# Kernel optimization log

Hardware: AMD Instinct MI355X
Metric: run time of the kernel (lower is better)

The kernel has to match this reference:

```python
import jax, jax.numpy as jnp
import numpy as np
import math

DIM = 4096
N_HEADS = 32
HEAD_DIM = DIM // N_HEADS
BSZ = 2
SEQLEN = 2048
MAX_SEQ = 2048


def _make_freqs_cis(seqlen, head_dim, theta=10000.0):
    # (seqlen, head_dim//2, 2) packed as (cos, sin) pairs, like complex rotary freqs
    inv = 1.0 / (theta ** (np.arange(0, head_dim, 2).astype(np.float32) / head_dim))
    t = np.arange(seqlen, dtype=np.float32)
    ang = np.outer(t, inv)  # (seqlen, head_dim//2)
    return jnp.asarray(np.stack([np.cos(ang), np.sin(ang)], axis=-1))


def setup_inputs() -> dict:
    key = jax.random.key(0)
    ks = jax.random.split(key, 6)
    scale = 1.0 / math.sqrt(DIM)
    x = jax.random.normal(ks[0], (BSZ, SEQLEN, DIM), dtype=jnp.float32)
    wq = jax.random.normal(ks[1], (DIM, DIM), dtype=jnp.float32) * scale
    wk = jax.random.normal(ks[2], (DIM, DIM), dtype=jnp.float32) * scale
    wv = jax.random.normal(ks[3], (DIM, DIM), dtype=jnp.float32) * scale
    wo = jax.random.normal(ks[4], (DIM, DIM), dtype=jnp.float32) * scale
    freqs_cis = _make_freqs_cis(SEQLEN, HEAD_DIM)
    # causal mask (1,1,S,S): 0 on/below diagonal, large negative above
    mask = jnp.triu(jnp.full((SEQLEN, SEQLEN), -1e9, dtype=jnp.float32), k=1)[None, None]
    hidden_state = jnp.zeros((2, BSZ, MAX_SEQ, N_HEADS, HEAD_DIM), dtype=jnp.float32)
    return {"x": x, "freqs_cis": freqs_cis, "mask": mask, "hidden_state": hidden_state,
            "wq": wq, "wk": wk, "wv": wv, "wo": wo, "start_pos": 0}


def _apply_rotary(x, freqs_cis):
    # x: (b, s, h, d); freqs_cis: (s, d//2, 2) as (cos, sin)
    b, s, h, d = x.shape
    xr = x.astype(jnp.float32).reshape(b, s, h, d // 2, 2)
    fc = freqs_cis.reshape(1, s, 1, d // 2, 2)
    real = xr[..., 0] * fc[..., 0] - xr[..., 1] * fc[..., 1]
    imag = xr[..., 0] * fc[..., 1] + xr[..., 1] * fc[..., 0]
    return jnp.stack([real, imag], axis=-1).reshape(b, s, h, d).astype(x.dtype)


def reference(x, freqs_cis, mask, hidden_state, wq, wk, wv, wo, start_pos):
    bsz, seqlen, dim = x.shape
    h, hd = N_HEADS, HEAD_DIM
    xq = (x @ wq.T).reshape(bsz, seqlen, h, hd)
    xk = (x @ wk.T).reshape(bsz, seqlen, h, hd)
    xv = (x @ wv.T).reshape(bsz, seqlen, h, hd)
    xq = _apply_rotary(xq, freqs_cis)
    xk = _apply_rotary(xk, freqs_cis)
    # KV-cache write at static start_pos
    new_k = hidden_state[0].at[:bsz, start_pos:start_pos + seqlen].set(xk)
    new_v = hidden_state[1].at[:bsz, start_pos:start_pos + seqlen].set(xv)
    new_hidden = jnp.stack([new_k, new_v], axis=0)
    keys = new_k[:bsz, :start_pos + seqlen]      # (b, kv, h, hd)
    values = new_v[:bsz, :start_pos + seqlen]
    # attention
    scores = jnp.einsum('bqhd,bkhd->bhqk', xq, keys) / math.sqrt(hd)
    scores = scores + mask
    probs = jax.nn.softmax(scores.astype(jnp.float32), axis=-1).astype(xq.dtype)
    out = jnp.einsum('bhqk,bkhd->bqhd', probs, values).reshape(bsz, seqlen, h * hd)
    return out @ wo.T, new_hidden
```

## Files before the change

kernel.cpp:

```cpp
#include <hip/hip_runtime.h>
#include <hip/hip_bf16.h>

#define DIM   4096
#define SEQ   2048
#define NH    32
#define HD    128
#define BSZ   2
#define SEG   16777216

typedef unsigned short u16;
typedef unsigned int   u32;
typedef __attribute__((ext_vector_type(8))) short bf16x8;
typedef __attribute__((ext_vector_type(4))) float f32x4;
typedef __attribute__((ext_vector_type(4))) u16   u16x4;

__device__ __forceinline__ float b2f(u16 u) {
    union { u32 i; float f; } c; c.i = ((u32)u) << 16; return c.f;
}
__device__ __forceinline__ u16 f2b(float f) {
    u32 x = __float_as_uint(f);
    return (u16)((x + 0x7FFFu + ((x >> 16) & 1u)) >> 16);
}
__device__ __forceinline__ void gload_lds16(const void* g, void* l) {
    __builtin_amdgcn_global_load_lds(
        (__attribute__((address_space(1))) void*)(unsigned long)(g),
        (__attribute__((address_space(3))) void*)(l), 16, 0, 0);
}

__global__ __launch_bounds__(256) void cast5(const float* __restrict__ x,
                                             const float* __restrict__ wq,
                                             const float* __restrict__ wk,
                                             const float* __restrict__ wv,
                                             const float* __restrict__ wo,
                                             u16* __restrict__ dst) {
    int i = blockIdx.x * 1024 + threadIdx.x * 4;
    int seg = i >> 24;
    int off = i & (SEG - 1);
    const float* s = x;
    if (seg == 1) s = wq; else if (seg == 2) s = wk;
    else if (seg == 3) s = wv; else if (seg == 4) s = wo;
    float4 v = *(const float4*)(s + off);
    u16x4 o; o.x = f2b(v.x); o.y = f2b(v.y); o.z = f2b(v.z); o.w = f2b(v.w);
    *(u16x4*)(dst + i) = o;
}

template<int OUT_BF16>
__global__ __launch_bounds__(256) void gemm_bt(const u16* __restrict__ A,
                                               const u16* __restrict__ Bbase,
                                               void* __restrict__ Cv) {
    __shared__ __align__(16) u16 smem[8192];
    const int tid = threadIdx.x;
    const int lane = tid & 63, w = tid >> 6;
    const int quad = lane >> 4, m16 = lane & 15;
    const int m0 = blockIdx.y * 128, n0 = blockIdx.x * 128;
    const int wm = (w & 1) * 64, wn = (w >> 1) * 64;
    const u16* B = Bbase + (size_t)blockIdx.z * SEG;

    f32x4 acc[4][4];
    for (int a = 0; a < 4; ++a) for (int b = 0; b < 4; ++b) acc[a][b] = 0.f;

    const int gbase = w * 256 + lane;

    for (int k0 = 0; k0 < DIM; k0 += 32) {
        __syncthreads();
        for (int j = 0; j < 4; ++j) {
            int g = gbase + j * 64;
            int row = (g >> 2) & 127;
            int ch = (g & 3) ^ ((row >> 1) & 3);
            const u16* src = (g < 512 ? A + (m0 + row) * DIM : B + (n0 + row) * DIM)
                             + k0 + ch * 8;
            gload_lds16(src, (char*)smem + w * 4096 + j * 1024);
        }
        __syncthreads();

        bf16x8 af[4], bfr[4];
        for (int mt = 0; mt < 4; ++mt) {
            int row = wm + mt * 16 + m16;
            int ch = quad ^ ((row >> 1) & 3);
            af[mt] = *(const bf16x8*)(smem + row * 32 + ch * 8);
        }
        for (int nt = 0; nt < 4; ++nt) {
            int row = wn + nt * 16 + m16;
            int ch = quad ^ ((row >> 1) & 3);
            bfr[nt] = *(const bf16x8*)(smem + 4096 + row * 32 + ch * 8);
        }
        for (int mt = 0; mt < 4; ++mt)
            for (int nt = 0; nt < 4; ++nt)
                acc[mt][nt] = __builtin_amdgcn_mfma_f32_16x16x32_bf16(
                    af[mt], bfr[nt], acc[mt][nt], 0, 0, 0);
    }

    for (int mt = 0; mt < 4; ++mt) for (int nt = 0; nt < 4; ++nt) {
        int row = m0 + wm + mt * 16 + quad * 4;
        int col = n0 + wn + nt * 16 + m16;
        if (OUT_BF16) {
            u16* C = (u16*)Cv + (size_t)blockIdx.z * SEG;
            for (int r = 0; r < 4; ++r) C[(row + r) * DIM + col] = f2b(acc[mt][nt][r]);
        } else {
            float* C = (float*)Cv + (size_t)blockIdx.z * SEG;
            for (int r = 0; r < 4; ++r) C[(row + r) * DIM + col] = acc[mt][nt][r];
        }
    }
}

__global__ __launch_bounds__(256) void rope(const u16* __restrict__ XQ,
                                            const u16* __restrict__ XK,
                                            const float* __restrict__ FC,
                                            u16* __restrict__ Qo,
                                            u16* __restrict__ Ko,
                                            float* __restrict__ KH) {
    int tid = blockIdx.x * 256 + threadIdx.x;
    int i = tid & 63;
    int s = (tid >> 11) & 2047;
    float2 cs = *(const float2*)(FC + (s * 64 + i) * 2);
    u32 q = ((const u32*)XQ)[tid];
    u32 k = ((const u32*)XK)[tid];
    float q0 = b2f((u16)(q & 0xffff)), q1 = b2f((u16)(q >> 16));
    float k0 = b2f((u16)(k & 0xffff)), k1 = b2f((u16)(k >> 16));
    float qr = q0 * cs.x - q1 * cs.y, qi = q0 * cs.y + q1 * cs.x;
    float kr = k0 * cs.x - k1 * cs.y, ki = k0 * cs.y + k1 * cs.x;
    ((u32*)Qo)[tid] = (u32)f2b(qr) | ((u32)f2b(qi) << 16);
    ((u32*)Ko)[tid] = (u32)f2b(kr) | ((u32)f2b(ki) << 16);
    *(float2*)(KH + (size_t)tid * 2) = make_float2(kr, ki);
}

__global__ __launch_bounds__(256) void vprep(const u16* __restrict__ XV,
                                             float* __restrict__ VH,
                                             u16* __restrict__ VT) {
    __shared__ u16 tile[64][65];
    int bs = blockIdx.x;
    int bd = blockIdx.y;
    int bh = blockIdx.z;
    int b = bh >> 5, h = bh & 31;
    int t = threadIdx.x;
    int c = t & 63, r4 = t >> 6;
    for (int i = 0; i < 16; ++i) {
        int sr = i * 4 + r4;
        int gi = ((b * SEQ + bs * 64 + sr) * NH + h) * HD + bd * 64 + c;
        u16 v = XV[gi];
        VH[gi] = b2f(v);
        tile[sr][c] = v;
    }
    __syncthreads();
    for (int i = 0; i < 16; ++i) {
        int dr = i * 4 + r4;
        VT[(bh * HD + bd * 64 + dr) * SEQ + bs * 64 + c] = tile[c][dr];
    }
}

__global__ __launch_bounds__(256, 2) void flash(const u16* __restrict__ Q,
                                                const u16* __restrict__ K,
                                                const u16* __restrict__ Vt,
                                                u16* __restrict__ O) {
    __shared__ __align__(16) u16 k_lds[64 * 128];
    __shared__ __align__(16) u16 v_lds[128 * 64];
    __shared__ __align__(16) u16 p_lds[4][32 * 68];

    const int tid = threadIdx.x, lane = tid & 63, w = tid >> 6;
    const int quad = lane >> 4, m16 = lane & 15;
    const int bh = blockIdx.x;
    const int b = bh >> 5, h = bh & 31;
    const int qt = (gridDim.y - 1) - blockIdx.y;
    const int q0 = qt * 128;
    const int wrow = q0 + w * 32;

    const int gk = w * 256 + lane;
    bf16x8 qa[2][4];
#pragma unroll
    for (int mt = 0; mt < 2; ++mt) {
        const u16* qp = Q + ((size_t)(b * SEQ + wrow + mt * 16 + m16) * NH + h) * HD;
#pragma unroll
        for (int ks = 0; ks < 4; ++ks) qa[mt][ks] = *(const bf16x8*)(qp + ks * 32 + quad * 8);
    }

    float mi[2][4], li[2][4];
    f32x4 o[2][8];
#pragma unroll
    for (int mt = 0; mt < 2; ++mt)
#pragma unroll
        for (int r = 0; r < 4; ++r) { mi[mt][r] = -1e30f; li[mt][r] = 0.f; }
#pragma unroll
    for (int mt = 0; mt < 2; ++mt)
#pragma unroll
        for (int n = 0; n < 8; ++n) o[mt][n] = 0.f;

    const float scale = 0.08838834764831845f;
    const int nkt = 2 * qt + 2;

    const u16* Kbase = K + ((size_t)(b * SEQ) * NH + h) * HD;
    const u16* Vbase = Vt + (size_t)(bh * HD) * SEQ;

    for (int kt = 0; kt < nkt; ++kt) {
        const int k0 = kt * 64;
        __syncthreads();
#pragma unroll
        for (int j = 0; j < 4; ++j) {
            int g = gk + j * 64;
            int r = g >> 4, p = g & 15, c = p ^ (r & 15);
            gload_lds16(Kbase + (size_t)(k0 + r) * DIM + c * 8,
                        (char*)k_lds + w * 4096 + j * 1024);
        }
#pragma unroll
        for (int j = 0; j < 4; ++j) {
            int g = gk + j * 64;
            int r = g >> 3, p = g & 7, c = p ^ (r & 7);
            gload_lds16(Vbase + (size_t)r * SEQ + k0 + c * 8,
                        (char*)v_lds + w * 4096 + j * 1024);
        }
        __syncthreads();

        if (k0 > wrow + 31) continue;

        f32x4 s[2][4];
#pragma unroll
        for (int mt = 0; mt < 2; ++mt)
#pragma unroll
            for (int nt = 0; nt < 4; ++nt) s[mt][nt] = 0.f;
#pragma unroll
        for (int ks = 0; ks < 4; ++ks)
#pragma unroll
            for (int nt = 0; nt < 4; ++nt) {
                int rk = nt * 16 + m16;
                int p = (ks * 4 + quad) ^ m16;
                bf16x8 kb = *(const bf16x8*)(k_lds + rk * 128 + p * 8);
#pragma unroll
                for (int mt = 0; mt < 2; ++mt)
                    s[mt][nt] = __builtin_amdgcn_mfma_f32_16x16x32_bf16(
                        qa[mt][ks], kb, s[mt][nt], 0, 0, 0);
            }

#pragma unroll
        for (int mt = 0; mt < 2; ++mt) {
            float sv[4][4];
            const bool need_mask = (k0 + 63) > (wrow + mt * 16);
#pragma unroll
            for (int nt = 0; nt < 4; ++nt)
#pragma unroll
                for (int r = 0; r < 4; ++r) {
                    float v = s[mt][nt][r] * scale;
                    if (need_mask) {
                        int col = k0 + nt * 16 + m16;
                        int rq = wrow + mt * 16 + quad * 4 + r;
                        if (col > rq) v = -1e30f;
                    }
                    sv[nt][r] = v;
                }
#pragma unroll
            for (int r = 0; r < 4; ++r) {
                float mx = fmaxf(fmaxf(sv[0][r], sv[1][r]), fmaxf(sv[2][r], sv[3][r]));
#pragma unroll
                for (int off = 8; off >= 1; off >>= 1) mx = fmaxf(mx, __shfl_xor(mx, off));
                float mnew = fmaxf(mi[mt][r], mx);
                float alpha = __expf(mi[mt][r] - mnew);
                float sum = 0.f;
#pragma unroll
                for (int nt = 0; nt < 4; ++nt) {
                    float pv = __expf(sv[nt][r] - mnew);
                    sum += pv;
                    p_lds[w][(mt * 16 + quad * 4 + r) * 68 + nt * 16 + m16] = f2b(pv);
                }
#pragma unroll
                for (int off = 8; off >= 1; off >>= 1) sum += __shfl_xor(sum, off);
                li[mt][r] = li[mt][r] * alpha + sum;
                mi[mt][r] = mnew;
#pragma unroll
                for (int n8 = 0; n8 < 8; ++n8) o[mt][n8][r] *= alpha;
            }
        }

        asm volatile("s_waitcnt lgkmcnt(0)" ::: "memory");

#pragma unroll
        for (int ks2 = 0; ks2 < 2; ++ks2) {
            bf16x8 pa[2];
#pragma unroll
            for (int mt = 0; mt < 2; ++mt)
                pa[mt] = *(const bf16x8*)(&p_lds[w][0] + (mt * 16 + m16) * 68 + ks2 * 32 + quad * 8);
#pragma unroll
            for (int n8 = 0; n8 < 8; ++n8) {
                int rv = n8 * 16 + m16;
                int p = (ks2 * 4 + quad) ^ (m16 & 7);
                bf16x8 vb = *(const bf16x8*)(v_lds + rv * 64 + p * 8);
#pragma unroll
                for (int mt = 0; mt < 2; ++mt)
                    o[mt][n8] = __builtin_amdgcn_mfma_f32_16x16x32_bf16(
                        pa[mt], vb, o[mt][n8], 0, 0, 0);
            }
        }
    }

#pragma unroll
    for (int mt = 0; mt < 2; ++mt) {
        float inv[4];
#pragma unroll
        for (int r = 0; r < 4; ++r) inv[r] = 1.0f / li[mt][r];
#pragma unroll
        for (int n8 = 0; n8 < 8; ++n8)
#pragma unroll
            for (int r = 0; r < 4; ++r) {
                int rq = wrow + mt * 16 + quad * 4 + r;
                O[((size_t)(b * SEQ + rq) * NH + h) * HD + n8 * 16 + m16] =
                    f2b(o[mt][n8][r] * inv[r]);
            }
    }
}

extern "C" void kernel_launch(void* const* d_in, const int* in_sizes, int n_in,
                              void* d_out, int out_size, void* d_ws, size_t ws_size,
                              hipStream_t stream) {
    const float* x  = (const float*)d_in[0];
    const float* fc = (const float*)d_in[1];
    const float* wq = (const float*)d_in[4];
    const float* wk = (const float*)d_in[5];
    const float* wv = (const float*)d_in[6];
    const float* wo = (const float*)d_in[7];

    float* out = (float*)d_out;
    float* kh  = out + 16777216;
    float* vh  = out + 33554432;

    u16* ws = (u16*)d_ws;
    u16* xb  = ws + 0L * SEG;
    u16* wqb = ws + 1L * SEG;
    u16* wkb = ws + 2L * SEG;
    u16* wvb = ws + 3L * SEG;
    u16* wob = ws + 4L * SEG;
    u16* xqb = ws + 5L * SEG;
    u16* xkb = ws + 6L * SEG;
    u16* xvb = ws + 7L * SEG;
    u16* qro = xb;
    u16* kro = wqb;
    u16* vt  = wkb;
    u16* ao  = wvb;

    cast5<<<dim3(81920), dim3(256), 0, stream>>>(x, wq, wk, wv, wo, ws);
    gemm_bt<1><<<dim3(32, 32, 3), dim3(256), 0, stream>>>(xb, wqb, (void*)xqb);
    rope<<<dim3(32768), dim3(256), 0, stream>>>(xqb, xkb, fc, qro, kro, kh);
    vprep<<<dim3(32, 2, 64), dim3(256), 0, stream>>>(xvb, vh, vt);
    flash<<<dim3(64, 16), dim3(256), 0, stream>>>(qro, kro, vt, ao);
    gemm_bt<0><<<dim3(32, 32, 1), dim3(256), 0, stream>>>(ao, wob, (void*)out);
}
```

Before: 1.343 ms.

## Replace GEMM with 256x256-tile 8-wave double-buffered pipelined kernel

Replaces the simple 128x128 single-buffer GEMM with a 512-thread kernel that computes 256x256 tiles with K-step 64. It double-buffers 128KB of LDS and interleaves global-to-LDS staging, LDS fragment loads and MFMA quadrants, using explicit waitcnt, barriers and setprio. The goal is to hide global-load latency and raise data reuse per block for the QKV and output projections. It risks lower occupancy from the large LDS footprint, and the hand-counted waitcnt values are fragile.

```diff
diff --git a/kernel.cpp b/kernel.cpp
--- a/kernel.cpp
+++ b/kernel.cpp
@@ -44,63 +44,157 @@
     *(u16x4*)(dst + i) = o;
 }
 
+#define BARRIER() do { asm volatile("" ::: "memory"); \
+                       __builtin_amdgcn_s_barrier(); \
+                       asm volatile("" ::: "memory"); } while (0)
+
 template<int OUT_BF16>
-__global__ __launch_bounds__(256) void gemm_bt(const u16* __restrict__ A,
-                                               const u16* __restrict__ Bbase,
-                                               void* __restrict__ Cv) {
-    __shared__ __align__(16) u16 smem[8192];
+__global__ __launch_bounds__(512, 2) void gemm8p(const u16* __restrict__ A,
+                                                 const u16* __restrict__ Bbase,
+                                                 void* __restrict__ Cv) {
+    __shared__ __align__(16) char lds[131072];
+
     const int tid = threadIdx.x;
     const int lane = tid & 63, w = tid >> 6;
     const int quad = lane >> 4, m16 = lane & 15;
-    const int m0 = blockIdx.y * 128, n0 = blockIdx.x * 128;
-    const int wm = (w & 1) * 64, wn = (w >> 1) * 64;
-    const u16* B = Bbase + (size_t)blockIdx.z * SEG;
-
-    f32x4 acc[4][4];
-    for (int a = 0; a < 4; ++a) for (int b = 0; b < 4; ++b) acc[a][b] = 0.f;
-
-    const int gbase = w * 256 + lane;
-
-    for (int k0 = 0; k0 < DIM; k0 += 32) {
-        __syncthreads();
-        for (int j = 0; j < 4; ++j) {
-            int g = gbase + j * 64;
-            int row = (g >> 2) & 127;
-            int ch = (g & 3) ^ ((row >> 1) & 3);
-            const u16* src = (g < 512 ? A + (m0 + row) * DIM : B + (n0 + row) * DIM)
-                             + k0 + ch * 8;
-            gload_lds16(src, (char*)smem + w * 4096 + j * 1024);
+    const int wm = w >> 2, wn = w & 3;
+    const int m0 = blockIdx.y * 256, n0 = blockIdx.x * 256;
+    const u16* Bp = Bbase + (size_t)blockIdx.z * SEG;
+
+    const u16* aSrc[2];
+    const u16* bSrc[2];
+#pragma unroll
+    for (int i = 0; i < 2; ++i) {
+        int p = i * 8192 + w * 1024 + lane * 16;
+        int q = p ^ (((p >> 8) & 3) << 4);
+        int rowoff = (q >> 11) * 16 + ((q >> 6) & 15);
+        int coloff = (((q >> 10) & 1) << 5) + ((q & 63) >> 1);
+        aSrc[i] = A  + (size_t)(m0 + rowoff) * DIM + coloff;
+        bSrc[i] = Bp + (size_t)(n0 + rowoff) * DIM + coloff;
+    }
+    const int laneoff = m16 * 64 + ((quad * 16) ^ (((m16 >> 2) & 3) << 4));
+
+    f32x4 acc[8][4];
+#pragma unroll
+    for (int a = 0; a < 8; ++a)
+#pragma unroll
+        for (int b = 0; b < 4; ++b) acc[a][b] = 0.f;
+
+    bf16x8 af[4][2];
+    bf16x8 bfr[4][2];
+
+#define STAGE_A(d, h, kt) do { int kk_ = ((kt) & 63) * 64;                       \
+    gload_lds16(aSrc[0] + (size_t)(h) * (128 * DIM) + kk_,                       \
+                lds + ((d) * 4 + (h)) * 16384 + w * 1024);                       \
+    gload_lds16(aSrc[1] + (size_t)(h) * (128 * DIM) + kk_,                       \
+                lds + ((d) * 4 + (h)) * 16384 + 8192 + w * 1024); } while (0)
+#define STAGE_B(d, h, kt) do { int kk_ = ((kt) & 63) * 64;                       \
+    gload_lds16(bSrc[0] + (size_t)(h) * (128 * DIM) + kk_,                       \
+                lds + ((d) * 4 + 2 + (h)) * 16384 + w * 1024);                   \
+    gload_lds16(bSrc[1] + (size_t)(h) * (128 * DIM) + kk_,                       \
+                lds + ((d) * 4 + 2 + (h)) * 16384 + 8192 + w * 1024); } while (0)
+#define LOAD_A(d, mh) do {                                                       \
+    const char* base_ = lds + ((d) * 4 + wm) * 16384 + (mh) * 8192 + laneoff;    \
+    _Pragma("unroll") for (int mt = 0; mt < 4; ++mt)                             \
+    _Pragma("unroll") for (int ks = 0; ks < 2; ++ks)                             \
+        af[mt][ks] = *(const bf16x8*)(base_ + mt * 2048 + ks * 1024); } while (0)
+#define LOAD_B(d, nh) do {                                                       \
+    const char* base_ = lds + ((d) * 4 + 2 + (wn >> 1)) * 16384                  \
+                        + (wn & 1) * 8192 + (nh) * 4096 + laneoff;               \
+    _Pragma("unroll") for (int nt = 0; nt < 2; ++nt)                             \
+    _Pragma("unroll") for (int ks = 0; ks < 2; ++ks)                             \
+        bfr[(nh) * 2 + nt][ks] = *(const bf16x8*)(base_ + nt * 2048 + ks * 1024);\
+    } while (0)
+#define MFMA_Q(mh, nh) do {                                                      \
+    _Pragma("unroll") for (int mt = 0; mt < 4; ++mt)                             \
+    _Pragma("unroll") for (int nt = 0; nt < 2; ++nt)                             \
+    _Pragma("unroll") for (int ks = 0; ks < 2; ++ks)                             \
+        acc[(mh) * 4 + mt][(nh) * 2 + nt] =                                      \
+            __builtin_amdgcn_mfma_f32_16x16x32_bf16(                             \
+                af[mt][ks], bfr[(nh) * 2 + nt][ks],                              \
+                acc[(mh) * 4 + mt][(nh) * 2 + nt], 0, 0, 0); } while (0)
+
+    STAGE_B(0, 0, 0); STAGE_B(0, 1, 0); STAGE_A(0, 0, 0); STAGE_A(0, 1, 0);
+    STAGE_B(1, 0, 1); STAGE_B(1, 1, 1);
+    asm volatile("s_waitcnt vmcnt(4)" ::: "memory");
+    BARRIER();
+
+    for (int it = 0; it < 32; ++it) {
+        const int t = 2 * it;
+        LOAD_A(0, 0); LOAD_B(0, 0);
+        STAGE_A(1, 0, t + 1);
+        asm volatile("s_waitcnt lgkmcnt(8)" ::: "memory");
+        BARRIER();
+        asm volatile("s_waitcnt lgkmcnt(0)" ::: "memory");
+        __builtin_amdgcn_s_setprio(1); MFMA_Q(0, 0); __builtin_amdgcn_s_setprio(0);
+        BARRIER();
+        LOAD_B(0, 1);
+        STAGE_A(1, 1, t + 1);
+        BARRIER();
+        asm volatile("s_waitcnt lgkmcnt(0)" ::: "memory");
+        __builtin_amdgcn_s_setprio(1); MFMA_Q(0, 1); __builtin_amdgcn_s_setprio(0);
+        BARRIER();
+        LOAD_A(0, 1);
+        STAGE_B(0, 0, t + 2);
+        BARRIER();
+        asm volatile("s_waitcnt lgkmcnt(0)" ::: "memory");
+        __builtin_amdgcn_s_setprio(1); MFMA_Q(1, 1); __builtin_amdgcn_s_setprio(0);
+        BARRIER();
+        STAGE_B(0, 1, t + 2);
+        BARRIER();
+        __builtin_amdgcn_s_setprio(1); MFMA_Q(1, 0); __builtin_amdgcn_s_setprio(0);
+        asm volatile("s_waitcnt vmcnt(4)" ::: "memory");
+        BARRIER();
+        LOAD_A(1, 0); LOAD_B(1, 0);
+        STAGE_A(0, 0, t + 2);
+        asm volatile("s_waitcnt lgkmcnt(8)" ::: "memory");
+        BARRIER();
+        asm volatile("s_waitcnt lgkmcnt(0)" ::: "memory");
+        __builtin_amdgcn_s_setprio(1); MFMA_Q(0, 0); __builtin_amdgcn_s_setprio(0);
+        BARRIER();
+        LOAD_B(1, 1);
+        STAGE_A(0, 1, t + 2);
+        BARRIER();
+        asm volatile("s_waitcnt lgkmcnt(0)" ::: "memory");
+        __builtin_amdgcn_s_setprio(1); MFMA_Q(0, 1); __builtin_amdgcn_s_setprio(0);
+        BARRIER();
+        LOAD_A(1, 1);
+        STAGE_B(1, 0, t + 3);
+        BARRIER();
+        asm volatile("s_waitcnt lgkmcnt(0)" ::: "memory");
+        __builtin_amdgcn_s_setprio(1); MFMA_Q(1, 1); __builtin_amdgcn_s_setprio(0);
+        BARRIER();
+        STAGE_B(1, 1, t + 3);
+        BARRIER();
+        __builtin_amdgcn_s_setprio(1); MFMA_Q(1, 0); __builtin_amdgcn_s_setprio(0);
+        asm volatile("s_waitcnt vmcnt(4)" ::: "memory");
+        BARRIER();
+    }
+    asm volatile("s_waitcnt vmcnt(0)" ::: "memory");
+
+#pragma unroll
+    for (int mt = 0; mt < 8; ++mt)
+#pragma unroll
+        for (int nt = 0; nt < 4; ++nt) {
+            const int row = m0 + wm * 128 + mt * 16 + quad * 4;
+            const int col = n0 + wn * 64 + nt * 16 + m16;
+            if (OUT_BF16) {
+                u16* C = (u16*)Cv + (size_t)blockIdx.z * SEG;
+#pragma unroll
+                for (int r = 0; r < 4; ++r)
+                    C[(size_t)(row + r) * DIM + col] = f2b(acc[mt][nt][r]);
+            } else {
+                float* C = (float*)Cv + (size_t)blockIdx.z * SEG;
+#pragma unroll
+                for (int r = 0; r < 4; ++r)
+                    C[(size_t)(row + r) * DIM + col] = acc[mt][nt][r];
+            }
         }
-        __syncthreads();
-
-        bf16x8 af[4], bfr[4];
-        for (int mt = 0; mt < 4; ++mt) {
-            int row = wm + mt * 16 + m16;
-            int ch = quad ^ ((row >> 1) & 3);
-            af[mt] = *(const bf16x8*)(smem + row * 32 + ch * 8);
-        }
-        for (int nt = 0; nt < 4; ++nt) {
-            int row = wn + nt * 16 + m16;
-            int ch = quad ^ ((row >> 1) & 3);
-            bfr[nt] = *(const bf16x8*)(smem + 4096 + row * 32 + ch * 8);
-        }
-        for (int mt = 0; mt < 4; ++mt)
-            for (int nt = 0; nt < 4; ++nt)
-                acc[mt][nt] = __builtin_amdgcn_mfma_f32_16x16x32_bf16(
-                    af[mt], bfr[nt], acc[mt][nt], 0, 0, 0);
-    }
-
-    for (int mt = 0; mt < 4; ++mt) for (int nt = 0; nt < 4; ++nt) {
-        int row = m0 + wm + mt * 16 + quad * 4;
-        int col = n0 + wn + nt * 16 + m16;
-        if (OUT_BF16) {
-            u16* C = (u16*)Cv + (size_t)blockIdx.z * SEG;
-            for (int r = 0; r < 4; ++r) C[(row + r) * DIM + col] = f2b(acc[mt][nt][r]);
-        } else {
-            float* C = (float*)Cv + (size_t)blockIdx.z * SEG;
-            for (int r = 0; r < 4; ++r) C[(row + r) * DIM + col] = acc[mt][nt][r];
-        }
-    }
+#undef STAGE_A
+#undef STAGE_B
+#undef LOAD_A
+#undef LOAD_B
+#undef MFMA_Q
 }
 
 __global__ __launch_bounds__(256) void rope(const u16* __restrict__ XQ,
@@ -334,9 +428,9 @@
     u16* ao  = wvb;
 
     cast5<<<dim3(81920), dim3(256), 0, stream>>>(x, wq, wk, wv, wo, ws);
-    gemm_bt<1><<<dim3(32, 32, 3), dim3(256), 0, stream>>>(xb, wqb, (void*)xqb);
+    gemm8p<1><<<dim3(16, 16, 3), dim3(512), 0, stream>>>(xb, wqb, (void*)xqb);
     rope<<<dim3(32768), dim3(256), 0, stream>>>(xqb, xkb, fc, qro, kro, kh);
     vprep<<<dim3(32, 2, 64), dim3(256), 0, stream>>>(xvb, vh, vt);
     flash<<<dim3(64, 16), dim3(256), 0, stream>>>(qro, kro, vt, ao);
-    gemm_bt<0><<<dim3(32, 32, 1), dim3(256), 0, stream>>>(ao, wob, (void*)out);
-}
+    gemm8p<0><<<dim3(16, 16, 1), dim3(512), 0, stream>>>(ao, wob, (void*)out);
+}
```

Result: faster. 1.149 ms (-14.5%).
